# Kernel tuning notes

Measured on AMD Instinct MI355X. Metric: run time of the kernel, lower is better.

Reference implementation:

```python
import math
import jax, jax.numpy as jnp
import numpy as np

B, I, G, C, D = 8192, 512, 32, 16, 32  # batch, dim_input, groups, num_components, dim_output
CD = C * D


def setup_inputs() -> dict:
    key = jax.random.key(0)
    ks = jax.random.split(key, 8)
    bound = 1.0 / math.sqrt(I)

    def unif(k, shape):
        return jax.random.uniform(k, shape, jnp.float32, -bound, bound)

    x = jax.random.normal(ks[0], (B, I), jnp.float32)
    # soft group-mixture weights (rows sum to 1, as produced upstream)
    g = jax.nn.softmax(jax.random.normal(ks[1], (B, G), jnp.float32), axis=-1)
    return {
        "x": x,
        "g": g,
        "W_mu": unif(ks[2], (G, I, CD)),
        "b_mu": unif(ks[3], (G, CD)),
        "W_sigma": unif(ks[4], (G, I, CD)),
        "b_sigma": unif(ks[5], (G, CD)),
        "W_pi": unif(ks[6], (G, I, C)),
        "b_pi": unif(ks[7], (G, C)),
    }


def _group_linear(x, g, W, b):
    # Fused form of: w_b = (g @ W.reshape(G, I*O)).reshape(B, I, O); x[:,None,:] @ w_b + g @ b
    # einsum avoids materializing the [B, I, O] per-sample weight tensor.
    return jnp.einsum("bi,gio,bg->bo", x, W, g) + g @ b


def reference(x, g, W_mu, b_mu, W_sigma, b_sigma, W_pi, b_pi):
    logits = _group_linear(x, g, W_pi, b_pi)                      # [B, C]
    loc = _group_linear(x, g, W_mu, b_mu)                         # [B, C*D]
    scale = jax.nn.softplus(_group_linear(x, g, W_sigma, b_sigma)) + 1e-7  # [B, C*D]
    # GroupGMM returns a MixtureSameFamily parameterized by (logits, loc, scale);
    # we return the concatenated parameter tensor [B, C + 2*C*D].
    return jnp.concatenate([logits, loc, scale], axis=-1)
```

## Files before the change

### kernel.cpp

```cpp
#include <hip/hip_runtime.h>
#include <hip/hip_bf16.h>

#define BATCH 8192
#define IDIM  512
#define GDIM  32
#define NOUT  1040
#define NPAD  1152
#define KW    16384
#define BM    128
#define BN    128
#define KQ    128

typedef short bf16x8 __attribute__((ext_vector_type(8)));
typedef float floatx4 __attribute__((ext_vector_type(4)));

__device__ inline unsigned pk2(float a, float b) {
    union { __hip_bfloat162 h2; unsigned u; } cv;
    cv.h2 = __float22bfloat162_rn(float2{a, b});
    return cv.u;
}

__global__ void cvt_bf16(const float* __restrict__ s, unsigned short* __restrict__ d) {
    int t = blockIdx.x * 256 + threadIdx.x;
    const float4* sp = (const float4*)s + (size_t)t * 2;
    float4 a = sp[0], b = sp[1];
    uint4 p;
    p.x = pk2(a.x, a.y); p.y = pk2(a.z, a.w);
    p.z = pk2(b.x, b.y); p.w = pk2(b.z, b.w);
    *(uint4*)(d + (size_t)t * 8) = p;
}

__global__ void prep_wt(const float* __restrict__ Wmu, const float* __restrict__ Wsig,
                        const float* __restrict__ Wpi, unsigned short* __restrict__ Wt) {
    int n = blockIdx.y * 256 + threadIdx.x;
    if (n >= NPAD) return;
    int k0 = blockIdx.x * 8;
    float v[8];
#pragma unroll
    for (int j = 0; j < 8; ++j) {
        int k = k0 + j, gg = k >> 9, i = k & 511;
        float val = 0.0f;
        if (n < 16)         val = Wpi [(gg * 512 + i) * 16  + n];
        else if (n < 528)   val = Wmu [(gg * 512 + i) * 512 + (n - 16)];
        else if (n < NOUT)  val = Wsig[(gg * 512 + i) * 512 + (n - 528)];
        v[j] = val;
    }
    uint4 p;
    p.x = pk2(v[0], v[1]); p.y = pk2(v[2], v[3]);
    p.z = pk2(v[4], v[5]); p.w = pk2(v[6], v[7]);
    const int col = n >> 7, r = n & 127;
    const int h = r >> 6, tn = (r >> 4) & 3, l15 = r & 15;
    const int kk = k0 >> 5, q = (k0 >> 3) & 3;
    size_t idx = ((size_t)(col * 512 + kk) << 12) + ((((h * 4 + tn) * 4 + q) * 16 + l15) * 8);
    *(uint4*)&Wt[idx] = p;
}

__global__ void prep_wb(const float* __restrict__ bmu, const float* __restrict__ bsig,
                        const float* __restrict__ bpi, unsigned short* __restrict__ Wb) {
    int n = blockIdx.y * 256 + threadIdx.x;
    if (n >= NPAD) return;
    int k0 = blockIdx.x * 8;
    float v[8];
#pragma unroll
    for (int j = 0; j < 8; ++j) {
        int gg = k0 + j;
        float val = 0.0f;
        if (n < 16)         val = bpi [gg * 16  + n];
        else if (n < 528)   val = bmu [gg * 512 + (n - 16)];
        else if (n < NOUT)  val = bsig[gg * 512 + (n - 528)];
        v[j] = val;
    }
    uint4 p;
    p.x = pk2(v[0], v[1]); p.y = pk2(v[2], v[3]);
    p.z = pk2(v[4], v[5]); p.w = pk2(v[6], v[7]);
    *(uint4*)&Wb[(size_t)n * GDIM + k0] = p;
}

__global__ __launch_bounds__(256, 2) void gemm_gmm(
        const unsigned short* __restrict__ xb, const unsigned short* __restrict__ gb,
        const float* __restrict__ g, const unsigned short* __restrict__ Wt,
        const unsigned short* __restrict__ Wb, float* __restrict__ out) {
    __shared__ unsigned short lA[BM * KQ];
    __shared__ float gsc[GDIM * BM];

    const int t = threadIdx.x, lane = t & 63, w = t >> 6;
    const int wm = (w & 1) * 64, wn = (w >> 1) * 64;
    const int q = lane >> 4, l15 = lane & 15;

    const int bx = blockIdx.x;
    const int seq = (bx & 7) * 72 + (bx >> 3);
    const int col = seq >> 6, mblk = seq & 63;
    const int m0 = mblk * BM, n0 = col * BN;

#pragma unroll
    for (int j = 0; j < 16; ++j) {
        int idx = t + 256 * j;
        int gg = idx >> 7, row = idx & 127;
        gsc[idx] = g[(size_t)(m0 + row) * GDIM + gg];
    }

    const unsigned short* Bbase = Wt + ((size_t)col * 512 << 12)
                                + (((wn >> 6) * 256 + lane) * 8);

    floatx4 acc[4][4] = {};
    floatx4 P[4][4] = {};
    uint4 breg[2][4];
    const int swA = l15 & 7;

    auto loadB = [&](int kk, int slot) {
        const unsigned kg = (((kk >> 2) & 31) * 16) + ((kk >> 7) * 4) + (kk & 3);
        const unsigned short* p = Bbase + ((size_t)kg << 12);
#pragma unroll
        for (int tn = 0; tn < 4; ++tn)
            breg[slot][tn] = *(const uint4*)(p + tn * 512);
    };

    loadB(0, 0);
    for (int kb = 0; kb < 4; ++kb) {
        __syncthreads();
        {
            const int r = t >> 1;
            const unsigned short* src = xb + (size_t)(m0 + r) * IDIM + kb * KQ + (t & 1) * 64;
#pragma unroll
            for (int j = 0; j < 8; ++j) {
                int gi = (t & 1) * 8 + j;
                uint4 v = *(const uint4*)(src + j * 8);
                *(uint4*)&lA[(r * 16 + (gi ^ (r & 7))) * 8] = v;
            }
        }
        __syncthreads();

        for (int gg = 0; gg < GDIM; ++gg) {
#pragma unroll
            for (int ks = 0; ks < 4; ++ks) {
                const int kk = ((kb * GDIM + gg) << 2) + ks;
                if (kk + 1 < 512) loadB(kk + 1, (kk + 1) & 1);
                bf16x8 af[4];
#pragma unroll
                for (int tm = 0; tm < 4; ++tm)
                    af[tm] = *(const bf16x8*)
                        &lA[((wm + tm * 16 + l15) * 16 + ((ks * 4 + q) ^ swA)) * 8];
                const int slot = kk & 1;
#pragma unroll
                for (int tm = 0; tm < 4; ++tm)
#pragma unroll
                    for (int tn = 0; tn < 4; ++tn)
                        P[tm][tn] = __builtin_amdgcn_mfma_f32_16x16x32_bf16(
                            af[tm], *(const bf16x8*)&breg[slot][tn], P[tm][tn], 0, 0, 0);
            }
#pragma unroll
            for (int tm = 0; tm < 4; ++tm) {
                floatx4 s4 = *(const floatx4*)&gsc[gg * BM + wm + tm * 16 + q * 4];
#pragma unroll
                for (int tn = 0; tn < 4; ++tn) {
#pragma unroll
                    for (int r = 0; r < 4; ++r)
                        acc[tm][tn][r] += s4[r] * P[tm][tn][r];
                    P[tm][tn] = (floatx4){0.f, 0.f, 0.f, 0.f};
                }
            }
        }
    }

    __syncthreads();
    {
        const int r = t >> 1;
        const unsigned short* src = gb + (size_t)(m0 + r) * GDIM + (t & 1) * 16;
        *(uint4*)&lA[r * 40 + (t & 1) * 16]     = *(const uint4*)(src);
        *(uint4*)&lA[r * 40 + (t & 1) * 16 + 8] = *(const uint4*)(src + 8);
    }
    __syncthreads();
    {
        bf16x8 afb[4], bb[4];
#pragma unroll
        for (int tm = 0; tm < 4; ++tm)
            afb[tm] = *(const bf16x8*)&lA[(wm + tm * 16 + l15) * 40 + q * 8];
#pragma unroll
        for (int tn = 0; tn < 4; ++tn)
            bb[tn] = *(const bf16x8*)(Wb + (size_t)(n0 + wn + tn * 16 + l15) * GDIM + q * 8);
#pragma unroll
        for (int tm = 0; tm < 4; ++tm)
#pragma unroll
            for (int tn = 0; tn < 4; ++tn)
                acc[tm][tn] = __builtin_amdgcn_mfma_f32_16x16x32_bf16(
                    afb[tm], bb[tn], acc[tm][tn], 0, 0, 0);
    }

#pragma unroll
    for (int tn = 0; tn < 4; ++tn) {
        int n = n0 + wn + tn * 16 + l15;
        if (n >= NOUT) continue;
        bool is_scale = (n >= 528);
#pragma unroll
        for (int tm = 0; tm < 4; ++tm) {
            int mbase = m0 + wm + tm * 16 + q * 4;
#pragma unroll
            for (int r = 0; r < 4; ++r) {
                float vv = acc[tm][tn][r];
                if (is_scale) {
                    float sp = (vv > 15.0f) ? vv : log1pf(expf(vv));
                    vv = sp + 1e-7f;
                }
                out[(size_t)(mbase + r) * NOUT + n] = vv;
            }
        }
    }
}

extern "C" void kernel_launch(void* const* d_in, const int* in_sizes, int n_in,
                              void* d_out, int out_size, void* d_ws, size_t ws_size,
                              hipStream_t stream) {
    const float* x    = (const float*)d_in[0];
    const float* g    = (const float*)d_in[1];
    const float* Wmu  = (const float*)d_in[2];
    const float* bmu  = (const float*)d_in[3];
    const float* Wsig = (const float*)d_in[4];
    const float* bsig = (const float*)d_in[5];
    const float* Wpi  = (const float*)d_in[6];
    const float* bpi  = (const float*)d_in[7];
    float* out = (float*)d_out;

    char* ws = (char*)d_ws;
    unsigned short* Wt = (unsigned short*)ws;  ws += (size_t)NPAD * KW * 2;
    unsigned short* xb = (unsigned short*)ws;  ws += (size_t)BATCH * IDIM * 2;
    unsigned short* gb = (unsigned short*)ws;  ws += (size_t)BATCH * GDIM * 2;
    unsigned short* Wb = (unsigned short*)ws;

    cvt_bf16<<<BATCH * IDIM / 2048, 256, 0, stream>>>(x, xb);
    cvt_bf16<<<BATCH * GDIM / 2048, 256, 0, stream>>>(g, gb);
    prep_wt<<<dim3(KW / 8, 5), 256, 0, stream>>>(Wmu, Wsig, Wpi, Wt);
    prep_wb<<<dim3(GDIM / 8, 5), 256, 0, stream>>>(bmu, bsig, bpi, Wb);
    gemm_gmm<<<(BATCH / BM) * (NPAD / BN), 256, 0, stream>>>(xb, gb, g, Wt, Wb, out);
}
```

Before: 563.1 us.

## Use prefix-sum trick on group accumulators and shrink N tile to 96

The per-group partial product P is no longer reset after each group. Instead the group weights are replaced by differences g[gg]-g[gg+1], so the running-sum accumulation gives the same result without zeroing P per group. The N tile shrinks from 128 to 96, with 3 MFMA columns per wave, a new weight layout and a launch bound of 3 blocks per SM, to cut register pressure and raise occupancy. The separate bf16 conversion of g is dropped and done inside the kernel instead. Differencing the weights may add rounding error, since the running P sums can grow large.

```diff
diff --git a/kernel.cpp b/kernel.cpp
--- a/kernel.cpp
+++ b/kernel.cpp
@@ -6,10 +6,10 @@
 #define GDIM  32
 #define NOUT  1040
 #define NPAD  1152
-#define KW    16384
 #define BM    128
-#define BN    128
+#define BN    96
 #define KQ    128
+#define SLAB  3072
 
 typedef short bf16x8 __attribute__((ext_vector_type(8)));
 typedef float floatx4 __attribute__((ext_vector_type(4)));
@@ -48,10 +48,10 @@
     uint4 p;
     p.x = pk2(v[0], v[1]); p.y = pk2(v[2], v[3]);
     p.z = pk2(v[4], v[5]); p.w = pk2(v[6], v[7]);
-    const int col = n >> 7, r = n & 127;
-    const int h = r >> 6, tn = (r >> 4) & 3, l15 = r & 15;
+    const int col = n / 96, r = n % 96;
+    const int h = r / 48, tn = (r >> 4) % 3, l15 = r & 15;
     const int kk = k0 >> 5, q = (k0 >> 3) & 3;
-    size_t idx = ((size_t)(col * 512 + kk) << 12) + ((((h * 4 + tn) * 4 + q) * 16 + l15) * 8);
+    size_t idx = (size_t)(col * 512 + kk) * SLAB + ((h * 3 + tn) * 4 + q) * 128 + l15 * 8;
     *(uint4*)&Wt[idx] = p;
 }
 
@@ -76,19 +76,19 @@
     *(uint4*)&Wb[(size_t)n * GDIM + k0] = p;
 }
 
-__global__ __launch_bounds__(256, 2) void gemm_gmm(
-        const unsigned short* __restrict__ xb, const unsigned short* __restrict__ gb,
-        const float* __restrict__ g, const unsigned short* __restrict__ Wt,
-        const unsigned short* __restrict__ Wb, float* __restrict__ out) {
+__global__ __launch_bounds__(256, 3) void gemm_gmm(
+        const unsigned short* __restrict__ xb, const float* __restrict__ g,
+        const unsigned short* __restrict__ Wt, const unsigned short* __restrict__ Wb,
+        float* __restrict__ out) {
     __shared__ unsigned short lA[BM * KQ];
     __shared__ float gsc[GDIM * BM];
 
     const int t = threadIdx.x, lane = t & 63, w = t >> 6;
-    const int wm = (w & 1) * 64, wn = (w >> 1) * 64;
+    const int wm = (w & 1) * 64, h = w >> 1, wn = h * 48;
     const int q = lane >> 4, l15 = lane & 15;
 
     const int bx = blockIdx.x;
-    const int seq = (bx & 7) * 72 + (bx >> 3);
+    const int seq = (bx & 7) * 96 + (bx >> 3);
     const int col = seq >> 6, mblk = seq & 63;
     const int m0 = mblk * BM, n0 = col * BN;
 
@@ -96,22 +96,23 @@
     for (int j = 0; j < 16; ++j) {
         int idx = t + 256 * j;
         int gg = idx >> 7, row = idx & 127;
-        gsc[idx] = g[(size_t)(m0 + row) * GDIM + gg];
-    }
-
-    const unsigned short* Bbase = Wt + ((size_t)col * 512 << 12)
-                                + (((wn >> 6) * 256 + lane) * 8);
-
-    floatx4 acc[4][4] = {};
-    floatx4 P[4][4] = {};
-    uint4 breg[2][4];
+        float a = g[(size_t)(m0 + row) * GDIM + gg];
+        float b = (gg < 31) ? g[(size_t)(m0 + row) * GDIM + gg + 1] : 0.0f;
+        gsc[idx] = a - b;
+    }
+
+    const unsigned short* Bbase = Wt + (size_t)col * 512 * SLAB
+                                + h * 1536 + q * 128 + l15 * 8;
+
+    floatx4 acc[4][3] = {};
+    uint4 breg[2][3];
     const int swA = l15 & 7;
 
     auto loadB = [&](int kk, int slot) {
         const unsigned kg = (((kk >> 2) & 31) * 16) + ((kk >> 7) * 4) + (kk & 3);
-        const unsigned short* p = Bbase + ((size_t)kg << 12);
-#pragma unroll
-        for (int tn = 0; tn < 4; ++tn)
+        const unsigned short* p = Bbase + (size_t)kg * SLAB;
+#pragma unroll
+        for (int tn = 0; tn < 3; ++tn)
             breg[slot][tn] = *(const uint4*)(p + tn * 512);
     };
 
@@ -130,6 +131,7 @@
         }
         __syncthreads();
 
+        floatx4 P[4][3] = {};
         for (int gg = 0; gg < GDIM; ++gg) {
 #pragma unroll
             for (int ks = 0; ks < 4; ++ks) {
@@ -144,7 +146,7 @@
 #pragma unroll
                 for (int tm = 0; tm < 4; ++tm)
 #pragma unroll
-                    for (int tn = 0; tn < 4; ++tn)
+                    for (int tn = 0; tn < 3; ++tn)
                         P[tm][tn] = __builtin_amdgcn_mfma_f32_16x16x32_bf16(
                             af[tm], *(const bf16x8*)&breg[slot][tn], P[tm][tn], 0, 0, 0);
             }
@@ -152,42 +154,41 @@
             for (int tm = 0; tm < 4; ++tm) {
                 floatx4 s4 = *(const floatx4*)&gsc[gg * BM + wm + tm * 16 + q * 4];
 #pragma unroll
-                for (int tn = 0; tn < 4; ++tn) {
+                for (int tn = 0; tn < 3; ++tn)
 #pragma unroll
                     for (int r = 0; r < 4; ++r)
                         acc[tm][tn][r] += s4[r] * P[tm][tn][r];
-                    P[tm][tn] = (floatx4){0.f, 0.f, 0.f, 0.f};
-                }
             }
         }
     }
 
+    __syncthreads();
+#pragma unroll
+    for (int j = 0; j < 16; ++j) {
+        int idx = t + 256 * j;
+        int gg = idx >> 7, row = idx & 127;
+        __hip_bfloat16 hb = __float2bfloat16(g[(size_t)(m0 + row) * GDIM + gg]);
+        lA[row * 40 + gg] = *(unsigned short*)&hb;
+    }
     __syncthreads();
     {
-        const int r = t >> 1;
-        const unsigned short* src = gb + (size_t)(m0 + r) * GDIM + (t & 1) * 16;
-        *(uint4*)&lA[r * 40 + (t & 1) * 16]     = *(const uint4*)(src);
-        *(uint4*)&lA[r * 40 + (t & 1) * 16 + 8] = *(const uint4*)(src + 8);
-    }
-    __syncthreads();
-    {
-        bf16x8 afb[4], bb[4];
+        bf16x8 afb[4], bb[3];
 #pragma unroll
         for (int tm = 0; tm < 4; ++tm)
             afb[tm] = *(const bf16x8*)&lA[(wm + tm * 16 + l15) * 40 + q * 8];
 #pragma unroll
-        for (int tn = 0; tn < 4; ++tn)
+        for (int tn = 0; tn < 3; ++tn)
             bb[tn] = *(const bf16x8*)(Wb + (size_t)(n0 + wn + tn * 16 + l15) * GDIM + q * 8);
 #pragma unroll
         for (int tm = 0; tm < 4; ++tm)
 #pragma unroll
-            for (int tn = 0; tn < 4; ++tn)
+            for (int tn = 0; tn < 3; ++tn)
                 acc[tm][tn] = __builtin_amdgcn_mfma_f32_16x16x32_bf16(
                     afb[tm], bb[tn], acc[tm][tn], 0, 0, 0);
     }
 
 #pragma unroll
-    for (int tn = 0; tn < 4; ++tn) {
+    for (int tn = 0; tn < 3; ++tn) {
         int n = n0 + wn + tn * 16 + l15;
         if (n >= NOUT) continue;
         bool is_scale = (n >= 528);
@@ -221,14 +222,12 @@
     float* out = (float*)d_out;
 
     char* ws = (char*)d_ws;
-    unsigned short* Wt = (unsigned short*)ws;  ws += (size_t)NPAD * KW * 2;
+    unsigned short* Wt = (unsigned short*)ws;  ws += (size_t)12 * 512 * SLAB * 2;
     unsigned short* xb = (unsigned short*)ws;  ws += (size_t)BATCH * IDIM * 2;
-    unsigned short* gb = (unsigned short*)ws;  ws += (size_t)BATCH * GDIM * 2;
     unsigned short* Wb = (unsigned short*)ws;
 
     cvt_bf16<<<BATCH * IDIM / 2048, 256, 0, stream>>>(x, xb);
-    cvt_bf16<<<BATCH * GDIM / 2048, 256, 0, stream>>>(g, gb);
-    prep_wt<<<dim3(KW / 8, 5), 256, 0, stream>>>(Wmu, Wsig, Wpi, Wt);
+    prep_wt<<<dim3(GDIM * IDIM / 8, 5), 256, 0, stream>>>(Wmu, Wsig, Wpi, Wt);
     prep_wb<<<dim3(GDIM / 8, 5), 256, 0, stream>>>(bmu, bsig, bpi, Wb);
-    gemm_gmm<<<(BATCH / BM) * (NPAD / BN), 256, 0, stream>>>(xb, gb, g, Wt, Wb, out);
-}
+    gemm_gmm<<<(BATCH / BM) * (NPAD / BN), 256, 0, stream>>>(xb, g, Wt, Wb, out);
+}
```

Result: slower. 774.6 us (+37.6%).
